# Performance work log

Hardware: AMD Instinct MI355X
Metric: run time of the kernel (lower is better)

Reference implementation:

```python
import jax, jax.numpy as jnp
import numpy as np

B = 65536
H = 1024          # hidden_dimension
D_OUT = 2         # output_dimension
N_EXPERTS = 10


def setup_inputs() -> dict:
    key = jax.random.key(0)
    ks = jax.random.split(key, 9)
    s = 0.02
    return {
        "x": jax.random.normal(ks[0], (B, 12), dtype=jnp.float32),
        "W1": jax.random.normal(ks[1], (H, 1), dtype=jnp.float32) * s,    # fc1 weight [out,in]
        "b1": jax.random.normal(ks[2], (H,), dtype=jnp.float32) * s,
        "Wmeta": jax.random.normal(ks[3], (N_EXPERTS, H), dtype=jnp.float32) * s,  # row i = fc_meta[i].weight[:,0]
        "bmeta": jax.random.normal(ks[4], (N_EXPERTS, H), dtype=jnp.float32) * s,  # row i = fc_meta[i].bias
        "W2": jax.random.normal(ks[5], (H, H), dtype=jnp.float32) * s,
        "b2": jax.random.normal(ks[6], (H,), dtype=jnp.float32) * s,
        "W3": jax.random.normal(ks[7], (D_OUT, H), dtype=jnp.float32) * s,
        "b3": jax.random.normal(ks[8], (D_OUT,), dtype=jnp.float32) * s,
    }


def reference(x, W1, b1, Wmeta, bmeta, W2, b2, W3, b3):
    one_hot = x[:, 0:10]          # [B, 10] expert selection weights
    delta = x[:, 10:11]           # [B, 1]
    phi = x[:, 11:12]             # [B, 1]
    # fc1(delta): [B,1] @ [1,H]
    x1 = delta * W1[:, 0] + b1    # [B, H]
    # expert i output: phi * Wmeta[i] + bmeta[i]; one-hot weighted sum over experts
    # sum_i one_hot[:,i]*(phi*Wmeta[i]+bmeta[i]) = phi*(one_hot@Wmeta) + one_hot@bmeta
    x2 = phi * (one_hot @ Wmeta) + one_hot @ bmeta  # [B, H]
    h = jax.nn.relu(x1 + x2)
    h = jax.nn.relu(h @ W2.T + b2)                  # fc2 + relu
    return h @ W3.T + b3                            # fc3 -> [B, 2]
```

## Files before the change

### kernel.cpp

```cpp
#include <hip/hip_runtime.h>
#include <stdint.h>

#define NROWS 65536
#define HD 1024
#define KT 32

typedef __attribute__((ext_vector_type(8))) short bf16x8;
typedef __attribute__((ext_vector_type(4))) float f32x4;

typedef __attribute__((address_space(1))) const unsigned int* gas_ptr;
typedef __attribute__((address_space(3))) unsigned int* las_ptr;

__device__ __forceinline__ unsigned short f2bf(float f) {
  union { float f; uint32_t u; } v; v.f = f;
  uint32_t u = v.u;
  return (unsigned short)((u + 0x7fffu + ((u >> 16) & 1u)) >> 16);
}

__device__ __forceinline__ void gl16(const void* g, void* l) {
  __builtin_amdgcn_global_load_lds((gas_ptr)g, (las_ptr)l, 16, 0, 0);
}

__global__ void k_w2bf(const float* __restrict__ W2, unsigned short* __restrict__ W2bf) {
  int i = blockIdx.x * 256 + threadIdx.x;
  int c = i >> 7, g = i & 127;
  const float4* s4 = (const float4*)(W2 + (size_t)c * HD + g * 8);
  float4 a = s4[0], b = s4[1];
  uint4 pk;
  pk.x = (uint32_t)f2bf(a.x) | ((uint32_t)f2bf(a.y) << 16);
  pk.y = (uint32_t)f2bf(a.z) | ((uint32_t)f2bf(a.w) << 16);
  pk.z = (uint32_t)f2bf(b.x) | ((uint32_t)f2bf(b.y) << 16);
  pk.w = (uint32_t)f2bf(b.z) | ((uint32_t)f2bf(b.w) << 16);
  int gs = (g & 124) | ((g & 3) ^ (c & 3));
  *(uint4*)(W2bf + (size_t)c * HD + gs * 8) = pk;
}

__global__ __launch_bounds__(512) void k_layer1(
    const float* __restrict__ x, const float* __restrict__ W1,
    const float* __restrict__ b1, const float* __restrict__ Wmeta,
    const float* __restrict__ bmeta, unsigned short* __restrict__ h) {
  __shared__ float xs[128 * 12];
  int r0 = blockIdx.x * 128;
  int t = threadIdx.x;
  int j0 = t * 2;
  float w1a = W1[j0], w1b = W1[j0 + 1];
  float b1a = b1[j0], b1b = b1[j0 + 1];
  float wma[10], wmb[10], bma[10], bmb[10];
#pragma unroll
  for (int e = 0; e < 10; e++) {
    float2 wmv = *(const float2*)(Wmeta + e * HD + j0);
    float2 bmv = *(const float2*)(bmeta + e * HD + j0);
    wma[e] = wmv.x; wmb[e] = wmv.y; bma[e] = bmv.x; bmb[e] = bmv.y;
  }
  for (int i = t; i < 128 * 12; i += 512) xs[i] = x[(size_t)r0 * 12 + i];
  __syncthreads();
  int g = j0 >> 3;
  for (int r = 0; r < 128; r++) {
    const float* xr = xs + r * 12;
    float delta = xr[10], phi = xr[11];
    float s1a = 0.f, s1b = 0.f, s2a = 0.f, s2b = 0.f;
#pragma unroll
    for (int e = 0; e < 10; e++) {
      float oh = xr[e];
      s1a = fmaf(oh, wma[e], s1a);
      s1b = fmaf(oh, wmb[e], s1b);
      s2a = fmaf(oh, bma[e], s2a);
      s2b = fmaf(oh, bmb[e], s2b);
    }
    float pa = fmaf(delta, w1a, b1a) + fmaf(phi, s1a, s2a);
    float pb = fmaf(delta, w1b, b1b) + fmaf(phi, s1b, s2b);
    pa = fmaxf(pa, 0.f); pb = fmaxf(pb, 0.f);
    uint32_t pk = (uint32_t)f2bf(pa) | ((uint32_t)f2bf(pb) << 16);
    int rr = r0 + r;
    int gs = (g & 124) | ((g & 3) ^ (rr & 3));
    *(uint32_t*)(h + (size_t)rr * HD + gs * 8 + (j0 & 7)) = pk;
  }
}

__global__ __launch_bounds__(256, 2) void k_gemm(
    const unsigned short* __restrict__ h, const unsigned short* __restrict__ W2bf,
    const float* __restrict__ b2, const float* __restrict__ W3,
    float* __restrict__ partial) {
  __shared__ char lds[73728];
  int tid = threadIdx.x;
  int b = (int)blockIdx.x;
  int bx = ((b & 7) << 8) | (b >> 3);
  int rt = bx >> 3, ct = bx & 7;
  size_t r0 = (size_t)rt * 256;
  int c0 = ct * 128;
  int w = tid >> 6, lane = tid & 63;
  int wm = w >> 1, wn = w & 1;
  int l15 = lane & 15, l4 = lane >> 4;
  int gsw = ((l4 ^ (l15 & 3)) << 4);
  int aBase = (wm * 128 + l15) * 64 + gsw;
  int bBase = (wn * 64 + l15) * 64 + gsw;

  f32x4 acc[8][4];
#pragma unroll
  for (int fm = 0; fm < 8; fm++)
#pragma unroll
    for (int fn = 0; fn < 4; fn++)
#pragma unroll
      for (int i = 0; i < 4; i++) acc[fm][fn][i] = 0.f;

  auto stage = [&](int T) {
    char* base = lds + (T % 3) * 24576;
    const unsigned short* hs = h + r0 * HD + T * 32;
    const unsigned short* ws = W2bf + (size_t)c0 * HD + T * 32;
#pragma unroll
    for (int q = 0; q < 4; q++) {
      int idx = tid + 256 * q;
      int row = idx >> 2, g4 = idx & 3;
      gl16(hs + (size_t)row * HD + g4 * 8, base + (size_t)idx * 16);
    }
#pragma unroll
    for (int q = 0; q < 2; q++) {
      int idx = tid + 256 * q;
      int row = idx >> 2, g4 = idx & 3;
      gl16(ws + (size_t)row * HD + g4 * 8, base + 16384 + (size_t)idx * 16);
    }
  };

  stage(0); stage(1);
  asm volatile("s_waitcnt vmcnt(6)" ::: "memory");
  __builtin_amdgcn_s_barrier();

  for (int T = 0; T < KT; T++) {
    const char* sA = lds + (T % 3) * 24576;
    const char* sB = sA + 16384;
    bf16x8 aF[4], bF[4];
#pragma unroll
    for (int i = 0; i < 4; i++) {
      aF[i] = *(const bf16x8*)(sA + aBase + i * 1024);
      bF[i] = *(const bf16x8*)(sB + bBase + i * 1024);
    }
    if (T < KT - 2) stage(T + 2);
    asm volatile("s_waitcnt lgkmcnt(0)" ::: "memory");
    __builtin_amdgcn_sched_barrier(0);
    __builtin_amdgcn_s_setprio(1);
#pragma unroll
    for (int fm = 0; fm < 4; fm++)
#pragma unroll
      for (int fn = 0; fn < 4; fn++)
        acc[fm][fn] = __builtin_amdgcn_mfma_f32_16x16x32_bf16(aF[fm], bF[fn], acc[fm][fn], 0, 0, 0);
    __builtin_amdgcn_s_setprio(0);
#pragma unroll
    for (int i = 0; i < 4; i++)
      aF[i] = *(const bf16x8*)(sA + aBase + (4 + i) * 1024);
    asm volatile("s_waitcnt lgkmcnt(0)" ::: "memory");
    __builtin_amdgcn_sched_barrier(0);
    __builtin_amdgcn_s_setprio(1);
#pragma unroll
    for (int fm = 0; fm < 4; fm++)
#pragma unroll
      for (int fn = 0; fn < 4; fn++)
        acc[4 + fm][fn] = __builtin_amdgcn_mfma_f32_16x16x32_bf16(aF[fm], bF[fn], acc[4 + fm][fn], 0, 0, 0);
    __builtin_amdgcn_s_setprio(0);
    if (T == KT - 2)      { asm volatile("s_waitcnt vmcnt(0)" ::: "memory"); }
    else if (T < KT - 2)  { asm volatile("s_waitcnt vmcnt(6)" ::: "memory"); }
    __builtin_amdgcn_s_barrier();
  }

  float b2c[4], w30[4], w31[4];
#pragma unroll
  for (int fn = 0; fn < 4; fn++) {
    int c = c0 + wn * 64 + fn * 16 + l15;
    b2c[fn] = b2[c];
    w30[fn] = W3[c];
    w31[fn] = W3[HD + c];
  }
  float* sOut = (float*)lds;
#pragma unroll
  for (int fm = 0; fm < 8; fm++) {
#pragma unroll
    for (int reg = 0; reg < 4; reg++) {
      float o0 = 0.f, o1 = 0.f;
#pragma unroll
      for (int fn = 0; fn < 4; fn++) {
        float v = fmaxf(acc[fm][fn][reg] + b2c[fn], 0.f);
        o0 = fmaf(v, w30[fn], o0);
        o1 = fmaf(v, w31[fn], o1);
      }
#pragma unroll
      for (int m = 1; m <= 8; m <<= 1) {
        o0 += __shfl_xor(o0, m);
        o1 += __shfl_xor(o1, m);
      }
      if (l15 == 0) {
        int row = wm * 128 + fm * 16 + l4 * 4 + reg;
        sOut[(wn * 256 + row) * 2 + 0] = o0;
        sOut[(wn * 256 + row) * 2 + 1] = o1;
      }
    }
  }
  __syncthreads();
#pragma unroll
  for (int q = 0; q < 2; q++) {
    int j = tid + q * 256;
    float s = sOut[j] + sOut[512 + j];
    partial[(size_t)ct * (NROWS * 2) + r0 * 2 + j] = s;
  }
}

__global__ void k_reduce(const float* __restrict__ partial, const float* __restrict__ b3,
                         float* __restrict__ out) {
  int i = blockIdx.x * 256 + threadIdx.x;
  float s = b3[i & 1];
#pragma unroll
  for (int ctt = 0; ctt < 8; ctt++) s += partial[(size_t)ctt * 131072 + i];
  out[i] = s;
}

extern "C" void kernel_launch(void* const* d_in, const int* in_sizes, int n_in,
                              void* d_out, int out_size, void* d_ws, size_t ws_size,
                              hipStream_t stream) {
  const float* x     = (const float*)d_in[0];
  const float* W1    = (const float*)d_in[1];
  const float* b1    = (const float*)d_in[2];
  const float* Wmeta = (const float*)d_in[3];
  const float* bmeta = (const float*)d_in[4];
  const float* W2    = (const float*)d_in[5];
  const float* b2    = (const float*)d_in[6];
  const float* W3    = (const float*)d_in[7];
  const float* b3    = (const float*)d_in[8];
  float* out = (float*)d_out;

  char* ws = (char*)d_ws;
  unsigned short* hbuf  = (unsigned short*)ws;
  unsigned short* W2bf  = (unsigned short*)(ws + (size_t)NROWS * HD * 2);
  float* partial = (float*)(ws + (size_t)NROWS * HD * 2 + (size_t)HD * HD * 2);

  k_w2bf<<<512, 256, 0, stream>>>(W2, W2bf);
  k_layer1<<<512, 512, 0, stream>>>(x, W1, b1, Wmeta, bmeta, hbuf);
  k_gemm<<<2048, 256, 0, stream>>>(hbuf, W2bf, b2, W3, partial);
  k_reduce<<<512, 256, 0, stream>>>(partial, b3, out);
}
```

Baseline: 216.0 us.

## Enlarge GEMM tile to 256x256 with 8 waves and double-buffered 64-wide K stages

The fc2 GEMM moves from 256x128 tiles with 4 waves and a triple-buffered K=32 pipeline to 256x256 tiles with 8 waves, 128KB dynamic LDS and a double-buffered K=64 pipeline. Each K step is split into sub-stages with interleaved loads and barriers. The larger column tile halves the number of column tiles, so less A traffic and fewer partial outputs go to the reduce kernel, which now sums 4 partials instead of 8. The cost is one block per CU at 128KB LDS and many more barriers per iteration, which may limit latency hiding.

```diff
diff --git a/kernel.cpp b/kernel.cpp
--- a/kernel.cpp
+++ b/kernel.cpp
@@ -3,7 +3,6 @@
 
 #define NROWS 65536
 #define HD 1024
-#define KT 32
 
 typedef __attribute__((ext_vector_type(8))) short bf16x8;
 typedef __attribute__((ext_vector_type(4))) float f32x4;
@@ -77,23 +76,23 @@
   }
 }
 
-__global__ __launch_bounds__(256, 2) void k_gemm(
+__global__ __launch_bounds__(512) void k_gemm(
     const unsigned short* __restrict__ h, const unsigned short* __restrict__ W2bf,
     const float* __restrict__ b2, const float* __restrict__ W3,
     float* __restrict__ partial) {
-  __shared__ char lds[73728];
+  extern __shared__ char lds[];
   int tid = threadIdx.x;
   int b = (int)blockIdx.x;
-  int bx = ((b & 7) << 8) | (b >> 3);
-  int rt = bx >> 3, ct = bx & 7;
+  int bx = ((b & 7) << 7) | (b >> 3);
+  int rt = bx >> 2, ct = bx & 3;
   size_t r0 = (size_t)rt * 256;
-  int c0 = ct * 128;
+  int c0 = ct * 256;
   int w = tid >> 6, lane = tid & 63;
-  int wm = w >> 1, wn = w & 1;
+  int wm = w >> 2, wn = w & 3;
   int l15 = lane & 15, l4 = lane >> 4;
-  int gsw = ((l4 ^ (l15 & 3)) << 4);
+  int gsw = (l4 ^ (l15 & 3)) << 4;
   int aBase = (wm * 128 + l15) * 64 + gsw;
-  int bBase = (wn * 64 + l15) * 64 + gsw;
+  int bBase = 32768 + (wn * 64 + l15) * 64 + gsw;
 
   f32x4 acc[8][4];
 #pragma unroll
@@ -103,63 +102,89 @@
 #pragma unroll
       for (int i = 0; i < 4; i++) acc[fm][fn][i] = 0.f;
 
-  auto stage = [&](int T) {
-    char* base = lds + (T % 3) * 24576;
-    const unsigned short* hs = h + r0 * HD + T * 32;
-    const unsigned short* ws = W2bf + (size_t)c0 * HD + T * 32;
-#pragma unroll
-    for (int q = 0; q < 4; q++) {
-      int idx = tid + 256 * q;
-      int row = idx >> 2, g4 = idx & 3;
-      gl16(hs + (size_t)row * HD + g4 * 8, base + (size_t)idx * 16);
-    }
-#pragma unroll
-    for (int q = 0; q < 2; q++) {
-      int idx = tid + 256 * q;
-      int row = idx >> 2, g4 = idx & 3;
-      gl16(ws + (size_t)row * HD + g4 * 8, base + 16384 + (size_t)idx * 16);
-    }
-  };
-
-  stage(0); stage(1);
-  asm volatile("s_waitcnt vmcnt(6)" ::: "memory");
+  const unsigned short* srcA0 = h    + (r0 + (tid >> 2)) * (size_t)HD + (tid & 3) * 8;
+  const unsigned short* srcB0 = W2bf + (size_t)(c0 + (tid >> 2)) * HD + (tid & 3) * 8;
+  const unsigned short* srcA1 = srcA0 + 128 * (size_t)HD;
+  const unsigned short* srcB1 = srcB0 + 128 * (size_t)HD;
+
+#define STAGE_A(T, ks)                                                              \
+  do {                                                                              \
+    char* dst = lds + ((T) & 1) * 65536 + (ks) * 16384 + (size_t)tid * 16;          \
+    gl16(srcA0 + (T) * 64 + (ks) * 32, dst);                                        \
+    gl16(srcA1 + (T) * 64 + (ks) * 32, dst + 8192);                                 \
+  } while (0)
+#define STAGE_B(T, ks)                                                              \
+  do {                                                                              \
+    char* dst = lds + ((T) & 1) * 65536 + 32768 + (ks) * 16384 + (size_t)tid * 16;  \
+    gl16(srcB0 + (T) * 64 + (ks) * 32, dst);                                        \
+    gl16(srcB1 + (T) * 64 + (ks) * 32, dst + 8192);                                 \
+  } while (0)
+
+#define MFMA16(MH)                                                                          \
+  do {                                                                                      \
+    __builtin_amdgcn_s_setprio(1);                                                          \
+    _Pragma("unroll")                                                                       \
+    for (int i = 0; i < 4; i++)                                                             \
+      _Pragma("unroll")                                                                     \
+      for (int j = 0; j < 4; j++)                                                           \
+        acc[(MH)*4 + i][j] =                                                                \
+            __builtin_amdgcn_mfma_f32_16x16x32_bf16(Af[i], Bf[j], acc[(MH)*4 + i][j], 0, 0, 0); \
+    __builtin_amdgcn_s_setprio(0);                                                          \
+  } while (0)
+
+  STAGE_A(0, 0); STAGE_B(0, 0); STAGE_A(0, 1); STAGE_B(0, 1);
+  asm volatile("s_waitcnt vmcnt(4)" ::: "memory");
   __builtin_amdgcn_s_barrier();
 
-  for (int T = 0; T < KT; T++) {
-    const char* sA = lds + (T % 3) * 24576;
-    const char* sB = sA + 16384;
-    bf16x8 aF[4], bF[4];
+#pragma unroll 2
+  for (int T = 0; T < 16; T++) {
+    int base = (T & 1) * 65536;
+    bf16x8 Af[4], Bf[4];
 #pragma unroll
     for (int i = 0; i < 4; i++) {
-      aF[i] = *(const bf16x8*)(sA + aBase + i * 1024);
-      bF[i] = *(const bf16x8*)(sB + bBase + i * 1024);
-    }
-    if (T < KT - 2) stage(T + 2);
-    asm volatile("s_waitcnt lgkmcnt(0)" ::: "memory");
-    __builtin_amdgcn_sched_barrier(0);
-    __builtin_amdgcn_s_setprio(1);
-#pragma unroll
-    for (int fm = 0; fm < 4; fm++)
-#pragma unroll
-      for (int fn = 0; fn < 4; fn++)
-        acc[fm][fn] = __builtin_amdgcn_mfma_f32_16x16x32_bf16(aF[fm], bF[fn], acc[fm][fn], 0, 0, 0);
-    __builtin_amdgcn_s_setprio(0);
+      Af[i] = *(const bf16x8*)(lds + base + aBase + i * 1024);
+      Bf[i] = *(const bf16x8*)(lds + base + bBase + i * 1024);
+    }
+    if (T < 15) STAGE_A(T + 1, 0);
+    __builtin_amdgcn_s_barrier();
+    asm volatile("s_waitcnt lgkmcnt(0)" ::: "memory");
+    __builtin_amdgcn_sched_barrier(0);
+    MFMA16(0);
+    __builtin_amdgcn_s_barrier();
 #pragma unroll
     for (int i = 0; i < 4; i++)
-      aF[i] = *(const bf16x8*)(sA + aBase + (4 + i) * 1024);
-    asm volatile("s_waitcnt lgkmcnt(0)" ::: "memory");
-    __builtin_amdgcn_sched_barrier(0);
-    __builtin_amdgcn_s_setprio(1);
-#pragma unroll
-    for (int fm = 0; fm < 4; fm++)
-#pragma unroll
-      for (int fn = 0; fn < 4; fn++)
-        acc[4 + fm][fn] = __builtin_amdgcn_mfma_f32_16x16x32_bf16(aF[fm], bF[fn], acc[4 + fm][fn], 0, 0, 0);
-    __builtin_amdgcn_s_setprio(0);
-    if (T == KT - 2)      { asm volatile("s_waitcnt vmcnt(0)" ::: "memory"); }
-    else if (T < KT - 2)  { asm volatile("s_waitcnt vmcnt(6)" ::: "memory"); }
-    __builtin_amdgcn_s_barrier();
-  }
+      Af[i] = *(const bf16x8*)(lds + base + aBase + 4096 + i * 1024);
+    if (T < 15) STAGE_B(T + 1, 0);
+    __builtin_amdgcn_s_barrier();
+    asm volatile("s_waitcnt lgkmcnt(0)" ::: "memory");
+    __builtin_amdgcn_sched_barrier(0);
+    MFMA16(1);
+    if (T == 15) { asm volatile("s_waitcnt vmcnt(0)" ::: "memory"); }
+    else         { asm volatile("s_waitcnt vmcnt(4)" ::: "memory"); }
+    __builtin_amdgcn_s_barrier();
+#pragma unroll
+    for (int i = 0; i < 4; i++) {
+      Af[i] = *(const bf16x8*)(lds + base + aBase + 16384 + i * 1024);
+      Bf[i] = *(const bf16x8*)(lds + base + bBase + 16384 + i * 1024);
+    }
+    if (T < 15) STAGE_A(T + 1, 1);
+    __builtin_amdgcn_s_barrier();
+    asm volatile("s_waitcnt lgkmcnt(0)" ::: "memory");
+    __builtin_amdgcn_sched_barrier(0);
+    MFMA16(0);
+    __builtin_amdgcn_s_barrier();
+#pragma unroll
+    for (int i = 0; i < 4; i++)
+      Af[i] = *(const bf16x8*)(lds + base + aBase + 4096 + 16384 + i * 1024);
+    if (T < 15) STAGE_B(T + 1, 1);
+    __builtin_amdgcn_s_barrier();
+    asm volatile("s_waitcnt lgkmcnt(0)" ::: "memory");
+    __builtin_amdgcn_sched_barrier(0);
+    MFMA16(1);
+    if (T < 15) { asm volatile("s_waitcnt vmcnt(4)" ::: "memory"); }
+    __builtin_amdgcn_s_barrier();
+  }
+  __syncthreads();
 
   float b2c[4], w30[4], w31[4];
 #pragma unroll
@@ -194,10 +219,9 @@
     }
   }
   __syncthreads();
-#pragma unroll
-  for (int q = 0; q < 2; q++) {
-    int j = tid + q * 256;
-    float s = sOut[j] + sOut[512 + j];
+  {
+    int j = tid;
+    float s = sOut[j] + sOut[512 + j] + sOut[1024 + j] + sOut[1536 + j];
     partial[(size_t)ct * (NROWS * 2) + r0 * 2 + j] = s;
   }
 }
@@ -207,7 +231,7 @@
   int i = blockIdx.x * 256 + threadIdx.x;
   float s = b3[i & 1];
 #pragma unroll
-  for (int ctt = 0; ctt < 8; ctt++) s += partial[(size_t)ctt * 131072 + i];
+  for (int ctt = 0; ctt < 4; ctt++) s += partial[(size_t)ctt * 131072 + i];
   out[i] = s;
 }
 
@@ -230,8 +254,10 @@
   unsigned short* W2bf  = (unsigned short*)(ws + (size_t)NROWS * HD * 2);
   float* partial = (float*)(ws + (size_t)NROWS * HD * 2 + (size_t)HD * HD * 2);
 
+  hipFuncSetAttribute((const void*)k_gemm, hipFuncAttributeMaxDynamicSharedMemorySize, 131072);
+
   k_w2bf<<<512, 256, 0, stream>>>(W2, W2bf);
   k_layer1<<<512, 512, 0, stream>>>(x, W1, b1, Wmeta, bmeta, hbuf);
-  k_gemm<<<2048, 256, 0, stream>>>(hbuf, W2bf, b2, W3, partial);
+  k_gemm<<<1024, 512, 131072, stream>>>(hbuf, W2bf, b2, W3, partial);
   k_reduce<<<512, 256, 0, stream>>>(partial, b3, out);
 }
```

After: 209.1 us. 1.03x faster.
